# Kernel tuning notes

Measured on AMD Instinct MI355X. Metric: run time of the kernel, lower is better.

The kernel has to match this reference:

```python
import jax, jax.numpy as jnp
import numpy as np

T, B, NINP, NHID = 1024, 64, 2048, 2048


def setup_inputs() -> dict:
    key = jax.random.key(0)
    ks = jax.random.split(key, 10)
    s = 0.02  # small init for numerical sanity (torch code used uniform(0,1))
    return {
        "x": jax.random.normal(ks[0], (T, B, NINP), dtype=jnp.float32),
        "hidden": jax.random.normal(ks[1], (B, NHID), dtype=jnp.float32),
        "W_cx": jax.random.normal(ks[2], (NHID, NINP), dtype=jnp.float32) * s,
        "W_ih": jax.random.normal(ks[3], (NHID, NHID), dtype=jnp.float32) * s,
        "W_ix": jax.random.normal(ks[4], (NHID, NINP), dtype=jnp.float32) * s,
        "W_fh": jax.random.normal(ks[5], (NHID, NHID), dtype=jnp.float32) * s,
        "W_fx": jax.random.normal(ks[6], (NHID, NINP), dtype=jnp.float32) * s,
        "b_i": jnp.zeros((NHID,), dtype=jnp.float32),
        "b_f": jnp.zeros((NHID,), dtype=jnp.float32),
    }


def reference(x, hidden, W_cx, W_ih, W_ix, W_fh, W_fx, b_i, b_f):
    # Precompute all input-side projections in big batched GEMMs (same math,
    # hoisted out of the sequential loop).
    content = jnp.einsum('tbi,hi->tbh', x, W_cx)            # [T,B,H]
    ix = jnp.einsum('tbi,hi->tbh', x, W_ix) + b_i            # [T,B,H]
    fx = jnp.einsum('tbi,hi->tbh', x, W_fx) + b_f            # [T,B,H]

    def step(h, inp):
        c_t, ix_t, fx_t = inp
        i_t = jax.nn.sigmoid(h @ W_ih.T + ix_t)
        f_t = jax.nn.sigmoid(h @ W_fh.T + fx_t)
        h_new = jnp.tanh(i_t * c_t + f_t * h)
        return h_new, h_new

    nexth, output = jax.lax.scan(step, hidden, (content, ix, fx))
    return output, nexth
```

## Files before the change

kernel.cpp:

```cpp
#include <hip/hip_runtime.h>
#include <cstdint>
#include <cstddef>

#define T_SEQ 1024
#define BATCH 64
#define NH 2048

typedef _Float16 half8 __attribute__((ext_vector_type(8)));
typedef _Float16 half4 __attribute__((ext_vector_type(4)));
typedef float f32x4 __attribute__((ext_vector_type(4)));
typedef unsigned u32x2 __attribute__((ext_vector_type(2)));

__device__ inline void gload_lds16(const void* g, void* l) {
    __builtin_amdgcn_global_load_lds(
        (const __attribute__((address_space(1))) uint32_t*)g,
        (__attribute__((address_space(3))) uint32_t*)l,
        16, 0, 0);
}

#define LLC_LD16(dst, base, OFFSTR)                                         \
    asm volatile("global_load_dwordx4 %0, %1, off offset:" OFFSTR " sc0 sc1" \
                 : "=v"(dst) : "v"(base))

#define LLC_ST2(addr, val)                                                   \
    asm volatile("global_store_short %0, %1, off sc0 sc1"                    \
                 :: "v"(addr), "v"(val) : "memory")

#define LLC_ST4(addr, val)                                                   \
    asm volatile("global_store_dword %0, %1, off sc0 sc1"                    \
                 :: "v"(addr), "v"(val) : "memory")
#define LLC_LD8(dst, addr)                                                   \
    asm volatile("global_load_dwordx2 %0, %1, off sc0 sc1\n\ts_waitcnt vmcnt(0)" \
                 : "=v"(dst) : "v"(addr))

__device__ inline void wait_vm0() {
    asm volatile("s_waitcnt vmcnt(0)" ::: "memory");
}

__global__ __launch_bounds__(256) void cvt_f32_f16(const float* __restrict__ src,
                                                   _Float16* __restrict__ dst,
                                                   long long n) {
    long long i = ((long long)blockIdx.x * 256 + threadIdx.x) * 4;
    long long stride = (long long)gridDim.x * 256 * 4;
    for (; i < n; i += stride) {
        const float4 v = *(const float4*)(src + i);
        half4 o;
        o[0] = (_Float16)v.x; o[1] = (_Float16)v.y;
        o[2] = (_Float16)v.z; o[3] = (_Float16)v.w;
        *(half4*)(dst + i) = o;
    }
}

__global__ __launch_bounds__(256) void proj_gemm(const _Float16* __restrict__ A,
                                                 const _Float16* __restrict__ B,
                                                 _Float16* __restrict__ C, int M) {
    __shared__ _Float16 As[128][64];
    __shared__ _Float16 Bs[128][64];
    const int NBN = 48;
    const int GH = 4;
    const int nbm = M >> 7;
    const int nwg = nbm * NBN;
    const int per = nwg >> 3;
    const int bid = blockIdx.x;
    const int swz = (bid & 7) * per + (bid >> 3);
    const int group = swz / (GH * NBN);
    const int rem = swz % (GH * NBN);
    const int bm = group * GH + (rem & (GH - 1));
    const int bn = rem / GH;

    const int tid = threadIdx.x;
    const int lane = tid & 63, w = tid >> 6;
    const int wm = w & 1, wn = w >> 1;

    f32x4 acc[4][4] = {};

    const int srow = lane >> 3;
    const int scol = (lane & 7) * 8;

    for (int bk = 0; bk < NH / 64; ++bk) {
#pragma unroll
        for (int i = 0; i < 4; ++i) {
            int r = w * 32 + i * 8;
            const _Float16* gA = A + (size_t)(bm * 128 + r + srow) * NH + bk * 64 + scol;
            gload_lds16(gA, &As[r][0]);
            const _Float16* gB = B + (size_t)(bn * 128 + r + srow) * NH + bk * 64 + scol;
            gload_lds16(gB, &Bs[r][0]);
        }
        __syncthreads();
#pragma unroll
        for (int kk = 0; kk < 2; ++kk) {
            half8 af[4], bf[4];
#pragma unroll
            for (int mi = 0; mi < 4; ++mi)
                af[mi] = *(const half8*)&As[wm * 64 + mi * 16 + (lane & 15)][kk * 32 + (lane >> 4) * 8];
#pragma unroll
            for (int ni = 0; ni < 4; ++ni)
                bf[ni] = *(const half8*)&Bs[wn * 64 + ni * 16 + (lane & 15)][kk * 32 + (lane >> 4) * 8];
#pragma unroll
            for (int mi = 0; mi < 4; ++mi)
#pragma unroll
                for (int ni = 0; ni < 4; ++ni)
                    acc[mi][ni] = __builtin_amdgcn_mfma_f32_16x16x32_f16(af[mi], bf[ni], acc[mi][ni], 0, 0, 0);
        }
        __syncthreads();
    }
#pragma unroll
    for (int mi = 0; mi < 4; ++mi)
#pragma unroll
        for (int ni = 0; ni < 4; ++ni)
#pragma unroll
            for (int r = 0; r < 4; ++r) {
                int m = bm * 128 + wm * 64 + mi * 16 + (lane >> 4) * 4 + r;
                int n = bn * 128 + wn * 64 + ni * 16 + (lane & 15);
                C[(size_t)m * 6144 + n] = (_Float16)acc[mi][ni][r];
            }
}

__global__ __launch_bounds__(512, 1) void scan_kernel(
    const _Float16* __restrict__ proj,
    const _Float16* __restrict__ Wr,
    _Float16* hb0, _Float16* hb1,
    const float* __restrict__ b_i, const float* __restrict__ b_f,
    float* __restrict__ out,
    unsigned* flags, int t0, int nsteps) {
    extern __shared__ char smem[];
    _Float16* Wlds = (_Float16*)smem;
    float* red = (float*)(smem + 131072);

    const int wg = blockIdx.x;
    const int xcd = wg & 7;
    const int slot = wg >> 3;
    const int g = slot & 1;
    const int idx = xcd * 16 + (slot >> 1);
    const int j0 = idx * 16;
    const int b0 = g * 32;
    unsigned* flags_g = flags + g * 256;

    const int tid = threadIdx.x;
    const int lane = tid & 63;
    const int w = tid >> 6;
    const int mi = w & 1;
    const int kq = w >> 1;

    for (int q = 0; q < 16; ++q) {
        int e = q * 512 + tid;
        int l = e & 63;
        int fk = (e >> 6) & 63;
        int gate = e >> 12;
        const _Float16* src = Wr + ((size_t)gate << 22) +
                              (size_t)(j0 + (l & 15)) * NH + fk * 32 + (l >> 4) * 8;
        *(half8*)(Wlds + ((size_t)(gate * 64 + fk) * 64 + l) * 8) = *(const half8*)src;
    }

    const float bi_s = b_i[j0 + (lane & 15)];
    const float bf_s = b_f[j0 + (lane & 15)];

    float hprev[4], pc[4], pix[4], pfx[4];
    if (kq == 0) {
        const _Float16* hini = (t0 & 1) ? hb1 : hb0;
#pragma unroll
        for (int r = 0; r < 4; ++r) {
            int b = b0 + mi * 16 + (lane >> 4) * 4 + r;
            int j = j0 + (lane & 15);
            unsigned tmp;
            asm volatile("global_load_ushort %0, %1, off sc0 sc1\n\ts_waitcnt vmcnt(0)"
                         : "=v"(tmp) : "v"(hini + (size_t)b * NH + j));
            hprev[r] = (float)__builtin_bit_cast(_Float16, (unsigned short)tmp);
            size_t pbase = ((size_t)b) * 6144 + j;
            pc[r] = (float)proj[pbase];
            pix[r] = (float)proj[pbase + 2048];
            pfx[r] = (float)proj[pbase + 4096];
        }
    }

    __syncthreads();

    for (int s = 0; s < nsteps; ++s) {
        const int t = t0 + s;
        const _Float16* hcur = (t & 1) ? hb1 : hb0;
        _Float16* hnxt = (t & 1) ? hb0 : hb1;

        half8 afr[16];
        const _Float16* hrow = hcur + (size_t)(b0 + mi * 16 + (lane & 15)) * NH +
                               kq * 512 + (lane >> 4) * 8;
        LLC_LD16(afr[0],  hrow, "0");
        LLC_LD16(afr[1],  hrow, "64");
        LLC_LD16(afr[2],  hrow, "128");
        LLC_LD16(afr[3],  hrow, "192");
        LLC_LD16(afr[4],  hrow, "256");
        LLC_LD16(afr[5],  hrow, "320");
        LLC_LD16(afr[6],  hrow, "384");
        LLC_LD16(afr[7],  hrow, "448");
        LLC_LD16(afr[8],  hrow, "512");
        LLC_LD16(afr[9],  hrow, "576");
        LLC_LD16(afr[10], hrow, "640");
        LLC_LD16(afr[11], hrow, "704");
        LLC_LD16(afr[12], hrow, "768");
        LLC_LD16(afr[13], hrow, "832");
        LLC_LD16(afr[14], hrow, "896");
        LLC_LD16(afr[15], hrow, "960");
        wait_vm0();
        __builtin_amdgcn_sched_barrier(0);

        f32x4 ai0 = {}, ai1 = {}, af0 = {}, af1 = {};
#pragma unroll
        for (int u = 0; u < 16; ++u) {
            int fk = kq * 16 + u;
            half8 wi = *(const half8*)(Wlds + ((size_t)fk * 64 + lane) * 8);
            half8 wf = *(const half8*)(Wlds + ((size_t)(64 + fk) * 64 + lane) * 8);
            if (u & 1) {
                ai1 = __builtin_amdgcn_mfma_f32_16x16x32_f16(afr[u], wi, ai1, 0, 0, 0);
                af1 = __builtin_amdgcn_mfma_f32_16x16x32_f16(afr[u], wf, af1, 0, 0, 0);
            } else {
                ai0 = __builtin_amdgcn_mfma_f32_16x16x32_f16(afr[u], wi, ai0, 0, 0, 0);
                af0 = __builtin_amdgcn_mfma_f32_16x16x32_f16(afr[u], wf, af0, 0, 0, 0);
            }
        }
        f32x4 acc_i = ai0 + ai1;
        f32x4 acc_f = af0 + af1;

        if (kq != 0) {
            const int sl = mi * 3 + (kq - 1);
#pragma unroll
            for (int r = 0; r < 4; ++r) {
                red[(sl * 8 + r) * 64 + lane] = acc_i[r];
                red[(sl * 8 + 4 + r) * 64 + lane] = acc_f[r];
            }
        }
        __syncthreads();

        float hn_keep[4];
        if (kq == 0) {
#pragma unroll
            for (int p = 0; p < 3; ++p) {
                const int sl = mi * 3 + p;
#pragma unroll
                for (int r = 0; r < 4; ++r) {
                    acc_i[r] += red[(sl * 8 + r) * 64 + lane];
                    acc_f[r] += red[(sl * 8 + 4 + r) * 64 + lane];
                }
            }
#pragma unroll
            for (int r = 0; r < 4; ++r) {
                int b = b0 + mi * 16 + (lane >> 4) * 4 + r;
                int j = j0 + (lane & 15);
                float iv = 1.0f / (1.0f + __expf(-(acc_i[r] + pix[r] + bi_s)));
                float fv = 1.0f / (1.0f + __expf(-(acc_f[r] + pfx[r] + bf_s)));
                float z = iv * pc[r] + fv * hprev[r];
                float hn = 1.0f - 2.0f / (__expf(2.0f * z) + 1.0f);
                hprev[r] = hn;
                hn_keep[r] = hn;
                _Float16 hn16 = (_Float16)hn;
                LLC_ST2(hnxt + (size_t)b * NH + j, hn16);
            }
            wait_vm0();
        }
        __syncthreads();

        const unsigned tv = (unsigned)(t + 1);
        if (tid == 0) {
            unsigned* myflag = flags_g + idx;
            LLC_ST4(myflag, tv);
        }
        if (kq == 0) {
#pragma unroll
            for (int r = 0; r < 4; ++r) {
                int b = b0 + mi * 16 + (lane >> 4) * 4 + r;
                int j = j0 + (lane & 15);
                out[(size_t)t * (BATCH * NH) + (size_t)b * NH + j] = hn_keep[r];
                if (t == T_SEQ - 1)
                    out[(size_t)T_SEQ * (BATCH * NH) + (size_t)b * NH + j] = hn_keep[r];
            }
            if (s + 1 < nsteps) {
#pragma unroll
                for (int r = 0; r < 4; ++r) {
                    int b = b0 + mi * 16 + (lane >> 4) * 4 + r;
                    int j = j0 + (lane & 15);
                    size_t pbase = ((size_t)(s + 1) * 64 + b) * 6144 + j;
                    pc[r] = (float)proj[pbase];
                    pix[r] = (float)proj[pbase + 2048];
                    pfx[r] = (float)proj[pbase + 4096];
                }
            }
        }
        if (w == 0) {
            const unsigned* fb = flags_g + lane * 2;
            while (true) {
                u32x2 v;
                LLC_LD8(v, fb);
                if (__all(v[0] >= tv && v[1] >= tv)) break;
                __builtin_amdgcn_s_sleep(1);
            }
        }
        __syncthreads();
    }
}

extern "C" void kernel_launch(void* const* d_in, const int* in_sizes, int n_in,
                              void* d_out, int out_size, void* d_ws, size_t ws_size,
                              hipStream_t stream) {
    const float* x = (const float*)d_in[0];
    const float* hidden = (const float*)d_in[1];
    const float* W_cx = (const float*)d_in[2];
    const float* W_ih = (const float*)d_in[3];
    const float* W_ix = (const float*)d_in[4];
    const float* W_fh = (const float*)d_in[5];
    const float* W_fx = (const float*)d_in[6];
    const float* b_i = (const float*)d_in[7];
    const float* b_f = (const float*)d_in[8];
    float* out = (float*)d_out;

    char* ws = (char*)d_ws;
    size_t off = 0;
    auto alloc = [&](size_t bytes) {
        char* p = ws + off;
        off += (bytes + 255) & ~(size_t)255;
        return p;
    };
    _Float16* Wp = (_Float16*)alloc((size_t)6144 * NH * 2);
    _Float16* Wr = (_Float16*)alloc((size_t)2 * NH * NH * 2);
    _Float16* hb0 = (_Float16*)alloc((size_t)BATCH * NH * 2);
    _Float16* hb1 = (_Float16*)alloc((size_t)BATCH * NH * 2);
    unsigned* flags = (unsigned*)alloc(4096);
    const size_t fixed = off;

    int chunk = 32;
    for (int c = T_SEQ; c >= 32; c >>= 1) {
        size_t need = fixed + (size_t)c * 64 * NH * 2 + (size_t)c * 64 * 6144 * 2 + 1024;
        if (need <= ws_size) { chunk = c; break; }
    }
    _Float16* xh = (_Float16*)alloc((size_t)chunk * 64 * NH * 2);
    _Float16* proj = (_Float16*)alloc((size_t)chunk * 64 * 6144 * 2);

    hipMemsetAsync(flags, 0, 4096, stream);

    const long long wsz = (long long)NH * NH;
    cvt_f32_f16<<<2048, 256, 0, stream>>>(W_cx, Wp, wsz);
    cvt_f32_f16<<<2048, 256, 0, stream>>>(W_ix, Wp + wsz, wsz);
    cvt_f32_f16<<<2048, 256, 0, stream>>>(W_fx, Wp + 2 * wsz, wsz);
    cvt_f32_f16<<<2048, 256, 0, stream>>>(W_ih, Wr, wsz);
    cvt_f32_f16<<<2048, 256, 0, stream>>>(W_fh, Wr + wsz, wsz);
    cvt_f32_f16<<<128, 256, 0, stream>>>(hidden, hb0, (long long)BATCH * NH);

    const int nch = T_SEQ / chunk;
    for (int c = 0; c < nch; ++c) {
        const int t0 = c * chunk;
        const int M = chunk * 64;
        cvt_f32_f16<<<2048, 256, 0, stream>>>(x + (size_t)t0 * 64 * NH, xh, (long long)M * NH);
        proj_gemm<<<dim3((M / 128) * 48), 256, 0, stream>>>(xh, Wp, proj, M);
        scan_kernel<<<256, 512, 143360, stream>>>(proj, Wr, hb0, hb1, b_i, b_f,
                                                  out, flags, t0, chunk);
    }
}
```

Measured before the change: 9.758 ms.

## Fuse input projections into scan kernel and relax inter-workgroup synchronization

Removes the separate projection GEMM and its large fp16 proj buffer. Each scan workgroup now holds its slice of the three input weight matrices in registers and computes the projections for step s+2 with MFMA while the recurrence runs, using a cross-wave LDS reduction. The h ping-pong becomes a 4-slot ring, and flags are split per batch half and per mi. Each wave polls only the flags it needs before loading h, instead of a whole-block barrier after publishing. This targets the proj write/read traffic and the barrier latency, but adds heavy register pressure (48 half8 weight fragments) and extra per-step MFMA work and x reads inside the latency-critical loop.

```diff
diff --git a/kernel.cpp b/kernel.cpp
--- a/kernel.cpp
+++ b/kernel.cpp
@@ -5,32 +5,23 @@
 #define T_SEQ 1024
 #define BATCH 64
 #define NH 2048
+#define HSZ (BATCH * NH)
 
 typedef _Float16 half8 __attribute__((ext_vector_type(8)));
 typedef _Float16 half4 __attribute__((ext_vector_type(4)));
 typedef float f32x4 __attribute__((ext_vector_type(4)));
-typedef unsigned u32x2 __attribute__((ext_vector_type(2)));
-
-__device__ inline void gload_lds16(const void* g, void* l) {
-    __builtin_amdgcn_global_load_lds(
-        (const __attribute__((address_space(1))) uint32_t*)g,
-        (__attribute__((address_space(3))) uint32_t*)l,
-        16, 0, 0);
-}
 
 #define LLC_LD16(dst, base, OFFSTR)                                         \
     asm volatile("global_load_dwordx4 %0, %1, off offset:" OFFSTR " sc0 sc1" \
                  : "=v"(dst) : "v"(base))
-
 #define LLC_ST2(addr, val)                                                   \
     asm volatile("global_store_short %0, %1, off sc0 sc1"                    \
                  :: "v"(addr), "v"(val) : "memory")
-
 #define LLC_ST4(addr, val)                                                   \
     asm volatile("global_store_dword %0, %1, off sc0 sc1"                    \
                  :: "v"(addr), "v"(val) : "memory")
-#define LLC_LD8(dst, addr)                                                   \
-    asm volatile("global_load_dwordx2 %0, %1, off sc0 sc1\n\ts_waitcnt vmcnt(0)" \
+#define LLC_LD4(dst, addr)                                                   \
+    asm volatile("global_load_dword %0, %1, off sc0 sc1\n\ts_waitcnt vmcnt(0)" \
                  : "=v"(dst) : "v"(addr))
 
 __device__ inline void wait_vm0() {
@@ -51,81 +42,19 @@
     }
 }
 
-__global__ __launch_bounds__(256) void proj_gemm(const _Float16* __restrict__ A,
-                                                 const _Float16* __restrict__ B,
-                                                 _Float16* __restrict__ C, int M) {
-    __shared__ _Float16 As[128][64];
-    __shared__ _Float16 Bs[128][64];
-    const int NBN = 48;
-    const int GH = 4;
-    const int nbm = M >> 7;
-    const int nwg = nbm * NBN;
-    const int per = nwg >> 3;
-    const int bid = blockIdx.x;
-    const int swz = (bid & 7) * per + (bid >> 3);
-    const int group = swz / (GH * NBN);
-    const int rem = swz % (GH * NBN);
-    const int bm = group * GH + (rem & (GH - 1));
-    const int bn = rem / GH;
-
-    const int tid = threadIdx.x;
-    const int lane = tid & 63, w = tid >> 6;
-    const int wm = w & 1, wn = w >> 1;
-
-    f32x4 acc[4][4] = {};
-
-    const int srow = lane >> 3;
-    const int scol = (lane & 7) * 8;
-
-    for (int bk = 0; bk < NH / 64; ++bk) {
-#pragma unroll
-        for (int i = 0; i < 4; ++i) {
-            int r = w * 32 + i * 8;
-            const _Float16* gA = A + (size_t)(bm * 128 + r + srow) * NH + bk * 64 + scol;
-            gload_lds16(gA, &As[r][0]);
-            const _Float16* gB = B + (size_t)(bn * 128 + r + srow) * NH + bk * 64 + scol;
-            gload_lds16(gB, &Bs[r][0]);
-        }
-        __syncthreads();
-#pragma unroll
-        for (int kk = 0; kk < 2; ++kk) {
-            half8 af[4], bf[4];
-#pragma unroll
-            for (int mi = 0; mi < 4; ++mi)
-                af[mi] = *(const half8*)&As[wm * 64 + mi * 16 + (lane & 15)][kk * 32 + (lane >> 4) * 8];
-#pragma unroll
-            for (int ni = 0; ni < 4; ++ni)
-                bf[ni] = *(const half8*)&Bs[wn * 64 + ni * 16 + (lane & 15)][kk * 32 + (lane >> 4) * 8];
-#pragma unroll
-            for (int mi = 0; mi < 4; ++mi)
-#pragma unroll
-                for (int ni = 0; ni < 4; ++ni)
-                    acc[mi][ni] = __builtin_amdgcn_mfma_f32_16x16x32_f16(af[mi], bf[ni], acc[mi][ni], 0, 0, 0);
-        }
-        __syncthreads();
-    }
-#pragma unroll
-    for (int mi = 0; mi < 4; ++mi)
-#pragma unroll
-        for (int ni = 0; ni < 4; ++ni)
-#pragma unroll
-            for (int r = 0; r < 4; ++r) {
-                int m = bm * 128 + wm * 64 + mi * 16 + (lane >> 4) * 4 + r;
-                int n = bn * 128 + wn * 64 + ni * 16 + (lane & 15);
-                C[(size_t)m * 6144 + n] = (_Float16)acc[mi][ni][r];
-            }
-}
-
 __global__ __launch_bounds__(512, 1) void scan_kernel(
-    const _Float16* __restrict__ proj,
+    const _Float16* __restrict__ xh,
     const _Float16* __restrict__ Wr,
-    _Float16* hb0, _Float16* hb1,
+    const _Float16* __restrict__ Wp,
+    _Float16* hslab,
     const float* __restrict__ b_i, const float* __restrict__ b_f,
     float* __restrict__ out,
-    unsigned* flags, int t0, int nsteps) {
+    unsigned* flags,
+    int t0, int nsteps) {
     extern __shared__ char smem[];
     _Float16* Wlds = (_Float16*)smem;
-    float* red = (float*)(smem + 131072);
+    float* red  = (float*)(smem + 131072);
+    float* red2 = (float*)(smem + 131072 + 12288);
 
     const int wg = blockIdx.x;
     const int xcd = wg & 7;
@@ -134,7 +63,6 @@
     const int idx = xcd * 16 + (slot >> 1);
     const int j0 = idx * 16;
     const int b0 = g * 32;
-    unsigned* flags_g = flags + g * 256;
 
     const int tid = threadIdx.x;
     const int lane = tid & 63;
@@ -152,36 +80,93 @@
         *(half8*)(Wlds + ((size_t)(gate * 64 + fk) * 64 + l) * 8) = *(const half8*)src;
     }
 
+    half8 wpf0[16], wpf1[16], wpf2[16];
+#pragma unroll
+    for (int u = 0; u < 16; ++u) {
+        const size_t coff = (size_t)(j0 + (lane & 15)) * NH + kq * 512 + u * 32 + (lane >> 4) * 8;
+        wpf0[u] = *(const half8*)(Wp + coff);
+        wpf1[u] = *(const half8*)(Wp + ((size_t)NH * NH) + coff);
+        wpf2[u] = *(const half8*)(Wp + 2 * ((size_t)NH * NH) + coff);
+    }
+
     const float bi_s = b_i[j0 + (lane & 15)];
     const float bf_s = b_f[j0 + (lane & 15)];
 
-    float hprev[4], pc[4], pix[4], pfx[4];
+    float hprev[4];
     if (kq == 0) {
-        const _Float16* hini = (t0 & 1) ? hb1 : hb0;
+        const _Float16* hini = hslab + (size_t)(t0 & 3) * HSZ;
 #pragma unroll
         for (int r = 0; r < 4; ++r) {
             int b = b0 + mi * 16 + (lane >> 4) * 4 + r;
-            int j = j0 + (lane & 15);
-            unsigned tmp;
-            asm volatile("global_load_ushort %0, %1, off sc0 sc1\n\ts_waitcnt vmcnt(0)"
-                         : "=v"(tmp) : "v"(hini + (size_t)b * NH + j));
-            hprev[r] = (float)__builtin_bit_cast(_Float16, (unsigned short)tmp);
-            size_t pbase = ((size_t)b) * 6144 + j;
-            pc[r] = (float)proj[pbase];
-            pix[r] = (float)proj[pbase + 2048];
-            pfx[r] = (float)proj[pbase + 4096];
-        }
-    }
+            hprev[r] = (float)hini[(size_t)b * NH + j0 + (lane & 15)];
+        }
+    }
+    float pcC[4], pixC[4], pfxC[4], pcN[4], pixN[4], pfxN[4];
 
     __syncthreads();
+
+#define PROJ_PASS(TT, PC_O, PIX_O, PFX_O)                                     \
+    {                                                                         \
+        f32x4 a0 = {}, a1 = {}, a2 = {};                                      \
+        const _Float16* xr = xh + ((size_t)(TT) * 64 + b0 + mi * 16 +         \
+                             (lane & 15)) * NH + kq * 512 + (lane >> 4) * 8;  \
+        _Pragma("unroll")                                                     \
+        for (int u = 0; u < 16; ++u) {                                        \
+            half8 xv = *(const half8*)(xr + u * 32);                          \
+            a0 = __builtin_amdgcn_mfma_f32_16x16x32_f16(xv, wpf0[u], a0, 0, 0, 0); \
+            a1 = __builtin_amdgcn_mfma_f32_16x16x32_f16(xv, wpf1[u], a1, 0, 0, 0); \
+            a2 = __builtin_amdgcn_mfma_f32_16x16x32_f16(xv, wpf2[u], a2, 0, 0, 0); \
+        }                                                                     \
+        if (kq != 0) {                                                        \
+            const int sl = mi * 3 + (kq - 1);                                 \
+            _Pragma("unroll")                                                 \
+            for (int r = 0; r < 4; ++r) {                                     \
+                red2[(sl * 12 + r) * 64 + lane] = a0[r];                      \
+                red2[(sl * 12 + 4 + r) * 64 + lane] = a1[r];                  \
+                red2[(sl * 12 + 8 + r) * 64 + lane] = a2[r];                  \
+            }                                                                 \
+        }                                                                     \
+        __syncthreads();                                                      \
+        if (kq == 0) {                                                        \
+            _Pragma("unroll")                                                 \
+            for (int p = 0; p < 3; ++p) {                                     \
+                const int sl = mi * 3 + p;                                    \
+                _Pragma("unroll")                                             \
+                for (int r = 0; r < 4; ++r) {                                 \
+                    a0[r] += red2[(sl * 12 + r) * 64 + lane];                 \
+                    a1[r] += red2[(sl * 12 + 4 + r) * 64 + lane];             \
+                    a2[r] += red2[(sl * 12 + 8 + r) * 64 + lane];             \
+                }                                                             \
+            }                                                                 \
+            _Pragma("unroll")                                                 \
+            for (int r = 0; r < 4; ++r) {                                     \
+                PC_O[r] = a0[r]; PIX_O[r] = a1[r]; PFX_O[r] = a2[r];          \
+            }                                                                 \
+        }                                                                     \
+        __syncthreads();                                                      \
+    }
+
+    PROJ_PASS(0, pcC, pixC, pfxC);
+    PROJ_PASS(1, pcN, pixN, pfxN);
 
     for (int s = 0; s < nsteps; ++s) {
         const int t = t0 + s;
-        const _Float16* hcur = (t & 1) ? hb1 : hb0;
-        _Float16* hnxt = (t & 1) ? hb0 : hb1;
+        const _Float16* hin = hslab + (size_t)(t & 3) * HSZ;
+        _Float16* hout = hslab + (size_t)((t + 1) & 3) * HSZ;
+        const unsigned tv = (unsigned)t;
+
+        {
+            const unsigned* fa = flags + (size_t)(g * 2 + mi) * 128 + kq * 32 + (lane & 31);
+            while (true) {
+                unsigned v;
+                LLC_LD4(v, fa);
+                if (__all((int)(v >= tv))) break;
+                __builtin_amdgcn_s_sleep(1);
+            }
+        }
 
         half8 afr[16];
-        const _Float16* hrow = hcur + (size_t)(b0 + mi * 16 + (lane & 15)) * NH +
+        const _Float16* hrow = hin + (size_t)(b0 + mi * 16 + (lane & 15)) * NH +
                                kq * 512 + (lane >> 4) * 8;
         LLC_LD16(afr[0],  hrow, "0");
         LLC_LD16(afr[1],  hrow, "64");
@@ -229,7 +214,6 @@
         }
         __syncthreads();
 
-        float hn_keep[4];
         if (kq == 0) {
 #pragma unroll
             for (int p = 0; p < 3; ++p) {
@@ -240,29 +224,23 @@
                     acc_f[r] += red[(sl * 8 + 4 + r) * 64 + lane];
                 }
             }
+            float hn_keep[4];
 #pragma unroll
             for (int r = 0; r < 4; ++r) {
                 int b = b0 + mi * 16 + (lane >> 4) * 4 + r;
                 int j = j0 + (lane & 15);
-                float iv = 1.0f / (1.0f + __expf(-(acc_i[r] + pix[r] + bi_s)));
-                float fv = 1.0f / (1.0f + __expf(-(acc_f[r] + pfx[r] + bf_s)));
-                float z = iv * pc[r] + fv * hprev[r];
+                float iv = 1.0f / (1.0f + __expf(-(acc_i[r] + pixC[r] + bi_s)));
+                float fv = 1.0f / (1.0f + __expf(-(acc_f[r] + pfxC[r] + bf_s)));
+                float z = iv * pcC[r] + fv * hprev[r];
                 float hn = 1.0f - 2.0f / (__expf(2.0f * z) + 1.0f);
                 hprev[r] = hn;
                 hn_keep[r] = hn;
                 _Float16 hn16 = (_Float16)hn;
-                LLC_ST2(hnxt + (size_t)b * NH + j, hn16);
+                LLC_ST2(hout + (size_t)b * NH + j, hn16);
             }
             wait_vm0();
-        }
-        __syncthreads();
-
-        const unsigned tv = (unsigned)(t + 1);
-        if (tid == 0) {
-            unsigned* myflag = flags_g + idx;
-            LLC_ST4(myflag, tv);
-        }
-        if (kq == 0) {
+            if (lane == 0)
+                LLC_ST4(flags + (size_t)(g * 2 + mi) * 128 + idx, (unsigned)(t + 1));
 #pragma unroll
             for (int r = 0; r < 4; ++r) {
                 int b = b0 + mi * 16 + (lane >> 4) * 4 + r;
@@ -271,28 +249,15 @@
                 if (t == T_SEQ - 1)
                     out[(size_t)T_SEQ * (BATCH * NH) + (size_t)b * NH + j] = hn_keep[r];
             }
-            if (s + 1 < nsteps) {
-#pragma unroll
-                for (int r = 0; r < 4; ++r) {
-                    int b = b0 + mi * 16 + (lane >> 4) * 4 + r;
-                    int j = j0 + (lane & 15);
-                    size_t pbase = ((size_t)(s + 1) * 64 + b) * 6144 + j;
-                    pc[r] = (float)proj[pbase];
-                    pix[r] = (float)proj[pbase + 2048];
-                    pfx[r] = (float)proj[pbase + 4096];
-                }
-            }
-        }
-        if (w == 0) {
-            const unsigned* fb = flags_g + lane * 2;
-            while (true) {
-                u32x2 v;
-                LLC_LD8(v, fb);
-                if (__all(v[0] >= tv && v[1] >= tv)) break;
-                __builtin_amdgcn_s_sleep(1);
-            }
-        }
-        __syncthreads();
+#pragma unroll
+            for (int r = 0; r < 4; ++r) {
+                pcC[r] = pcN[r]; pixC[r] = pixN[r]; pfxC[r] = pfxN[r];
+            }
+        }
+
+        if (s + 2 < nsteps) {
+            PROJ_PASS(s + 2, pcN, pixN, pfxN);
+        }
     }
 }
 
@@ -317,20 +282,18 @@
         off += (bytes + 255) & ~(size_t)255;
         return p;
     };
-    _Float16* Wp = (_Float16*)alloc((size_t)6144 * NH * 2);
+    _Float16* Wp = (_Float16*)alloc((size_t)3 * NH * NH * 2);
     _Float16* Wr = (_Float16*)alloc((size_t)2 * NH * NH * 2);
-    _Float16* hb0 = (_Float16*)alloc((size_t)BATCH * NH * 2);
-    _Float16* hb1 = (_Float16*)alloc((size_t)BATCH * NH * 2);
+    _Float16* hslab = (_Float16*)alloc((size_t)4 * HSZ * 2);
     unsigned* flags = (unsigned*)alloc(4096);
     const size_t fixed = off;
 
     int chunk = 32;
     for (int c = T_SEQ; c >= 32; c >>= 1) {
-        size_t need = fixed + (size_t)c * 64 * NH * 2 + (size_t)c * 64 * 6144 * 2 + 1024;
+        size_t need = fixed + (size_t)c * 64 * NH * 2 + 1024;
         if (need <= ws_size) { chunk = c; break; }
     }
     _Float16* xh = (_Float16*)alloc((size_t)chunk * 64 * NH * 2);
-    _Float16* proj = (_Float16*)alloc((size_t)chunk * 64 * 6144 * 2);
 
     hipMemsetAsync(flags, 0, 4096, stream);
 
@@ -340,15 +303,14 @@
     cvt_f32_f16<<<2048, 256, 0, stream>>>(W_fx, Wp + 2 * wsz, wsz);
     cvt_f32_f16<<<2048, 256, 0, stream>>>(W_ih, Wr, wsz);
     cvt_f32_f16<<<2048, 256, 0, stream>>>(W_fh, Wr + wsz, wsz);
-    cvt_f32_f16<<<128, 256, 0, stream>>>(hidden, hb0, (long long)BATCH * NH);
+    cvt_f32_f16<<<128, 256, 0, stream>>>(hidden, hslab, (long long)BATCH * NH);
 
     const int nch = T_SEQ / chunk;
     for (int c = 0; c < nch; ++c) {
         const int t0 = c * chunk;
         const int M = chunk * 64;
         cvt_f32_f16<<<2048, 256, 0, stream>>>(x + (size_t)t0 * 64 * NH, xh, (long long)M * NH);
-        proj_gemm<<<dim3((M / 128) * 48), 256, 0, stream>>>(xh, Wp, proj, M);
-        scan_kernel<<<256, 512, 143360, stream>>>(proj, Wr, hb0, hb1, b_i, b_f,
+        scan_kernel<<<256, 512, 161792, stream>>>(xh, Wr, Wp, hslab, b_i, b_f,
                                                   out, flags, t0, chunk);
     }
 }
```

Measured after the change: 16.88 ms. +72.9%, slower.
